# Performance work log

Measured on AMD Instinct MI355X. Metric: run time of the kernel, lower is better.

The kernel has to match this reference:

```python
import jax, jax.numpy as jnp
import numpy as np

N = 100000   # nodes
E = 1600000  # edges
IN = 512     # in_channels
H = 256      # hidden_channels
C = 40       # out_channels
BITS = 8     # INT8 fake quantization


def fake_quant(x, bits=BITS):
    """Symmetric per-tensor quantize-dequantize with straight-through estimator."""
    qmax = float(2 ** (bits - 1) - 1)
    scale = jnp.max(jnp.abs(x)) / qmax + 1e-12
    q = jnp.clip(jnp.round(x / scale), -qmax - 1.0, qmax) * scale
    # STE: forward = q, backward = identity
    return x + jax.lax.stop_gradient(q - x)


def quant_linear(x, w, b):
    # LinearQuantized: fake-quant inputs and weights, fp accumulate
    return fake_quant(x) @ fake_quant(w).T + b


def gcn_propagate(x, edge_index):
    """Symmetric-normalized sparse propagation: out = D^-1/2 A D^-1/2 x."""
    src, dst = edge_index[0], edge_index[1]
    deg = jax.ops.segment_sum(jnp.ones((E,), x.dtype), dst, num_segments=N)
    dinv = jnp.where(deg > 0, jax.lax.rsqrt(jnp.maximum(deg, 1.0)), 0.0)
    coef = dinv[src] * dinv[dst]                     # [E]
    msgs = x[src] * coef[:, None]                    # [E, C]
    return jax.ops.segment_sum(msgs, dst, num_segments=N)  # [N, C]


def setup_inputs() -> dict:
    key = jax.random.key(0)
    ks = jax.random.split(key, 6)
    x = jax.random.normal(ks[0], (N, IN), jnp.float32)
    edge_index = jax.random.randint(ks[1], (2, E), 0, N, dtype=jnp.int32)
    w1 = jax.random.normal(ks[2], (H, IN), jnp.float32) * (1.0 / np.sqrt(IN))
    b1 = jnp.zeros((H,), jnp.float32)
    w2 = jax.random.normal(ks[3], (C, H), jnp.float32) * (1.0 / np.sqrt(H))
    b2 = jnp.zeros((C,), jnp.float32)
    return {"x": x, "edge_index": edge_index, "w1": w1, "b1": b1, "w2": w2, "b2": b2}


def reference(x, edge_index, w1, b1, w2, b2):
    # dropout: identity in eval mode
    h = jax.nn.relu(quant_linear(x, w1, b1))         # [N, H]
    z = quant_linear(h, w2, b2)                      # [N, C]
    z = gcn_propagate(z, edge_index)                 # [N, C]
    return jax.nn.log_softmax(z, axis=1)
```

## Files before the change

kernel.cpp:

```cpp
#include <hip/hip_runtime.h>
#include <hip/hip_bf16.h>
#include <stdint.h>
#include <stddef.h>

#define NN   100000
#define NE   1600000
#define INC  512
#define HID  256
#define OC   40
#define OCP  48

#define LDK  72
#define LDB2 264

#define NBKT ((NN + 255) / 256)

typedef __bf16 bf16_t;
typedef __bf16 bf16x8 __attribute__((ext_vector_type(8)));
typedef __bf16 bf16x4 __attribute__((ext_vector_type(4)));
typedef float  f32x4  __attribute__((ext_vector_type(4)));

__device__ unsigned g_amax_bits[4];
__device__ float    g_dinv[NN];
__device__ bf16_t   g_qw1[HID * INC];
__device__ bf16_t   g_qw2[OCP * HID];
__device__ float    g_h[(size_t)NN * HID];
__device__ float    g_z[(size_t)NN * OC];
__device__ unsigned g_chist[NBKT];
__device__ unsigned g_cstart[NBKT + 1];
__device__ unsigned g_ccur[NBKT];
__device__ uint2    g_bin[NE];
__device__ unsigned g_rowstart[NN + 1];
__device__ int      g_csr_src[NE];

__device__ __forceinline__ bf16_t quant1(float v, float rs) {
    return (bf16_t)fminf(fmaxf(rintf(v * rs), -128.0f), 127.0f);
}

__global__ void init_kernel() {
    int idx = blockIdx.x * blockDim.x + threadIdx.x;
    int stride = gridDim.x * blockDim.x;
    for (int i = idx; i < NBKT; i += stride) g_chist[i] = 0u;
    for (int i = idx; i < OCP * HID; i += stride) g_qw2[i] = (bf16_t)0.0f;
    if (idx < 4) g_amax_bits[idx] = 0u;
}

__global__ void chist_kernel(const int* __restrict__ ei) {
    const int* dst = ei + NE;
    __shared__ unsigned hist[NBKT];
    int t = threadIdx.x;
    for (int i = t; i < NBKT; i += 256) hist[i] = 0u;
    __syncthreads();
    int idx = blockIdx.x * 256 + t;
    int stride = gridDim.x * 256;
    for (int e = idx; e < NE; e += stride) atomicAdd(&hist[dst[e] >> 8], 1u);
    __syncthreads();
    for (int i = t; i < NBKT; i += 256) {
        unsigned c = hist[i];
        if (c) atomicAdd(&g_chist[i], c);
    }
}

__global__ void cscan_kernel() {
    int t = threadIdx.x;
    unsigned v = (t < NBKT) ? g_chist[t] : 0u;
    int lane = t & 63, wv = t >> 6;
    unsigned sc = v;
#pragma unroll
    for (int off = 1; off < 64; off <<= 1) {
        unsigned n = __shfl_up(sc, off, 64);
        if (lane >= off) sc += n;
    }
    __shared__ unsigned ws[8];
    if (lane == 63) ws[wv] = sc;
    __syncthreads();
    unsigned woff = 0;
    for (int w = 0; w < 8; w++) if (w < wv) woff += ws[w];
    unsigned excl = woff + sc - v;
    if (t < NBKT) { g_cstart[t] = excl; g_ccur[t] = excl; }
    if (t == 0) g_cstart[NBKT] = NE;
}

#define BIN_BLOCKS 200
#define BIN_EPB    (NE / BIN_BLOCKS)
__global__ void bin_kernel(const int* __restrict__ ei) {
    const int* srcp = ei;
    const int* dstp = ei + NE;
    __shared__ unsigned hist[NBKT];
    __shared__ unsigned base[NBKT];
    int t = threadIdx.x;
    int e0 = blockIdx.x * BIN_EPB, e1 = e0 + BIN_EPB;
    for (int i = t; i < NBKT; i += 256) hist[i] = 0u;
    __syncthreads();
    for (int e = e0 + t; e < e1; e += 256) atomicAdd(&hist[dstp[e] >> 8], 1u);
    __syncthreads();
    for (int i = t; i < NBKT; i += 256) {
        unsigned c = hist[i];
        base[i] = c ? atomicAdd(&g_ccur[i], c) : 0u;
        hist[i] = 0u;
    }
    __syncthreads();
    for (int e = e0 + t; e < e1; e += 256) {
        int d = dstp[e], s = srcp[e];
        int b = d >> 8;
        unsigned r = atomicAdd(&hist[b], 1u);
        g_bin[base[b] + r] = make_uint2((unsigned)s, (unsigned)d);
    }
}

__global__ void local_kernel() {
    int b = blockIdx.x, t = threadIdx.x;
    unsigned e0 = g_cstart[b], e1 = g_cstart[b + 1];
    __shared__ unsigned hist[256];
    __shared__ unsigned curs[256];
    __shared__ unsigned wsum[4];
    hist[t] = 0u;
    __syncthreads();
    for (unsigned e = e0 + t; e < e1; e += 256) atomicAdd(&hist[g_bin[e].y & 255], 1u);
    __syncthreads();
    unsigned v = hist[t];
    int lane = t & 63, wv = t >> 6;
    unsigned sc = v;
#pragma unroll
    for (int off = 1; off < 64; off <<= 1) {
        unsigned n = __shfl_up(sc, off, 64);
        if (lane >= off) sc += n;
    }
    if (lane == 63) wsum[wv] = sc;
    __syncthreads();
    unsigned woff = 0;
    for (int w = 0; w < 4; w++) if (w < wv) woff += wsum[w];
    unsigned excl = woff + sc - v;
    int node = b * 256 + t;
    if (node < NN) {
        g_rowstart[node] = e0 + excl;
        g_dinv[node] = v ? rsqrtf((float)v) : 0.0f;
    }
    if (b == 0 && t == 0) g_rowstart[NN] = NE;
    curs[t] = excl;
    __syncthreads();
    for (unsigned e = e0 + t; e < e1; e += 256) {
        uint2 ed = g_bin[e];
        unsigned r = atomicAdd(&curs[ed.y & 255], 1u);
        g_csr_src[e0 + r] = (int)ed.x;
    }
}

__global__ void absmax_kernel(const float* __restrict__ src, int n4, int slot) {
    int idx = blockIdx.x * blockDim.x + threadIdx.x;
    int stride = gridDim.x * blockDim.x;
    const f32x4* s4 = (const f32x4*)src;
    float m = 0.0f;
    for (int i = idx; i < n4; i += stride) {
        f32x4 v = s4[i];
        m = fmaxf(m, fmaxf(fmaxf(fabsf(v.x), fabsf(v.y)),
                           fmaxf(fabsf(v.z), fabsf(v.w))));
    }
#pragma unroll
    for (int off = 32; off > 0; off >>= 1) m = fmaxf(m, __shfl_xor(m, off, 64));
    __shared__ float sm[4];
    if ((threadIdx.x & 63) == 0) sm[threadIdx.x >> 6] = m;
    __syncthreads();
    if (threadIdx.x == 0) {
        float mm = fmaxf(fmaxf(sm[0], sm[1]), fmaxf(sm[2], sm[3]));
        atomicMax(&g_amax_bits[slot], __float_as_uint(mm));
    }
}

__global__ void quantw_kernel(const float* __restrict__ src, int n4, int slot, int which) {
    bf16_t* dst = which ? g_qw2 : g_qw1;
    float rs = 1.0f / (__uint_as_float(g_amax_bits[slot]) / 127.0f + 1e-12f);
    int idx = blockIdx.x * blockDim.x + threadIdx.x;
    int stride = gridDim.x * blockDim.x;
    const f32x4* s4 = (const f32x4*)src;
    bf16x4* d4 = (bf16x4*)dst;
    for (int i = idx; i < n4; i += stride) {
        f32x4 v = s4[i];
        bf16x4 o;
        o[0] = quant1(v.x, rs); o[1] = quant1(v.y, rs);
        o[2] = quant1(v.z, rs); o[3] = quant1(v.w, rs);
        d4[i] = o;
    }
}

__launch_bounds__(256)
__global__ void gemm1_kernel(const float* __restrict__ x, const float* __restrict__ b1) {
    __shared__ bf16_t lA[128 * LDK];
    __shared__ bf16_t lB[128 * LDK];
    int t = threadIdx.x;
    int mtile = blockIdx.x >> 1, ntile = blockIdx.x & 1;
    int lane = t & 63, wv = t >> 6;
    int quad = lane >> 4, l16 = lane & 15;
    int mq = wv >> 1, nq = wv & 1;

    float scale_x = __uint_as_float(g_amax_bits[0]) / 127.0f + 1e-12f;
    float rs = 1.0f / scale_x;

    int srow = t >> 3;
    int sch  = t & 7;

    const float*  xbase[4];
    const bf16_t* wbase[4];
#pragma unroll
    for (int p = 0; p < 4; p++) {
        int gr = mtile * 128 + p * 32 + srow; if (gr >= NN) gr = NN - 1;
        xbase[p] = x + (size_t)gr * INC + sch * 8;
        wbase[p] = g_qw1 + (size_t)(ntile * 128 + p * 32 + srow) * INC + sch * 8;
    }

    f32x4 acc[4][4] = {};
#pragma unroll 1
    for (int kit = 0; kit < 8; kit++) {
        __syncthreads();
#pragma unroll
        for (int p = 0; p < 4; p++) {
            int row = p * 32 + srow;
            f32x4 v0 = *(const f32x4*)(xbase[p] + kit * 64);
            f32x4 v1 = *(const f32x4*)(xbase[p] + kit * 64 + 4);
            bf16x8 bb = *(const bf16x8*)(wbase[p] + kit * 64);
            bf16x8 o;
            o[0] = quant1(v0.x, rs); o[1] = quant1(v0.y, rs);
            o[2] = quant1(v0.z, rs); o[3] = quant1(v0.w, rs);
            o[4] = quant1(v1.x, rs); o[5] = quant1(v1.y, rs);
            o[6] = quant1(v1.z, rs); o[7] = quant1(v1.w, rs);
            *(bf16x8*)(lA + row * LDK + sch * 8) = o;
            *(bf16x8*)(lB + row * LDK + sch * 8) = bb;
        }
        __syncthreads();
#pragma unroll
        for (int k32 = 0; k32 < 2; k32++) {
            int cs = (k32 * 4 + quad) * 8;
            bf16x8 a[4], b[4];
#pragma unroll
            for (int i = 0; i < 4; i++)
                a[i] = *(const bf16x8*)(lA + (mq * 64 + i * 16 + l16) * LDK + cs);
#pragma unroll
            for (int j = 0; j < 4; j++)
                b[j] = *(const bf16x8*)(lB + (nq * 64 + j * 16 + l16) * LDK + cs);
#pragma unroll
            for (int i = 0; i < 4; i++)
#pragma unroll
                for (int j = 0; j < 4; j++)
                    acc[i][j] = __builtin_amdgcn_mfma_f32_16x16x32_bf16(a[i], b[j], acc[i][j], 0, 0, 0);
        }
    }
    float s = scale_x * (__uint_as_float(g_amax_bits[1]) / 127.0f + 1e-12f);
    float lmax = 0.0f;
#pragma unroll
    for (int j = 0; j < 4; j++) {
        int col = ntile * 128 + nq * 64 + j * 16 + l16;
        float bias = b1[col];
#pragma unroll
        for (int i = 0; i < 4; i++) {
#pragma unroll
            for (int r = 0; r < 4; r++) {
                int grow = mtile * 128 + mq * 64 + i * 16 + quad * 4 + r;
                float v = fmaxf(s * acc[i][j][r] + bias, 0.0f);
                lmax = fmaxf(lmax, v);
                if (grow < NN) g_h[(size_t)grow * HID + col] = v;
            }
        }
    }
#pragma unroll
    for (int off = 32; off > 0; off >>= 1) lmax = fmaxf(lmax, __shfl_xor(lmax, off, 64));
    if (lane == 0) atomicMax(&g_amax_bits[3], __float_as_uint(lmax));
}

__launch_bounds__(256)
__global__ void gemm2_kernel(const float* __restrict__ b2) {
    __shared__ bf16_t lB2[OCP * LDB2];
    __shared__ bf16_t lA2[128 * LDK];
    int t = threadIdx.x;
    int mtile = blockIdx.x;
    int lane = t & 63, wv = t >> 6;
    int quad = lane >> 4, l16 = lane & 15;

#pragma unroll
    for (int p = 0; p < 6; p++) {
        int ci = p * 256 + t;
        int row = ci >> 5, ch = ci & 31;
        *(bf16x8*)(lB2 + row * LDB2 + ch * 8) =
            *(const bf16x8*)(g_qw2 + row * 256 + ch * 8);
    }

    float scale_h = __uint_as_float(g_amax_bits[3]) / 127.0f + 1e-12f;
    float rs = 1.0f / scale_h;
    int srow = t >> 3, sch = t & 7;
    const float* hbase[4];
#pragma unroll
    for (int p = 0; p < 4; p++) {
        int gr = mtile * 128 + p * 32 + srow; if (gr >= NN) gr = NN - 1;
        hbase[p] = g_h + (size_t)gr * HID + sch * 8;
    }

    f32x4 acc[2][3] = {};
#pragma unroll 1
    for (int kit = 0; kit < 4; kit++) {
        if (kit) __syncthreads();
#pragma unroll
        for (int p = 0; p < 4; p++) {
            int row = p * 32 + srow;
            f32x4 v0 = *(const f32x4*)(hbase[p] + kit * 64);
            f32x4 v1 = *(const f32x4*)(hbase[p] + kit * 64 + 4);
            bf16x8 o;
            o[0] = quant1(v0.x, rs); o[1] = quant1(v0.y, rs);
            o[2] = quant1(v0.z, rs); o[3] = quant1(v0.w, rs);
            o[4] = quant1(v1.x, rs); o[5] = quant1(v1.y, rs);
            o[6] = quant1(v1.z, rs); o[7] = quant1(v1.w, rs);
            *(bf16x8*)(lA2 + row * LDK + sch * 8) = o;
        }
        __syncthreads();
#pragma unroll
        for (int k32 = 0; k32 < 2; k32++) {
            int csA = (k32 * 4 + quad) * 8;
            int chB = (kit * 8 + k32 * 4 + quad) * 8;
            bf16x8 a[2], b[3];
#pragma unroll
            for (int i = 0; i < 2; i++)
                a[i] = *(const bf16x8*)(lA2 + (wv * 32 + i * 16 + l16) * LDK + csA);
#pragma unroll
            for (int j = 0; j < 3; j++)
                b[j] = *(const bf16x8*)(lB2 + (j * 16 + l16) * LDB2 + chB);
#pragma unroll
            for (int i = 0; i < 2; i++)
#pragma unroll
                for (int j = 0; j < 3; j++)
                    acc[i][j] = __builtin_amdgcn_mfma_f32_16x16x32_bf16(a[i], b[j], acc[i][j], 0, 0, 0);
        }
    }
    float s = scale_h * (__uint_as_float(g_amax_bits[2]) / 127.0f + 1e-12f);
#pragma unroll
    for (int j = 0; j < 3; j++) {
        int col = j * 16 + l16;
        float bias = (col < OC) ? b2[col] : 0.0f;
#pragma unroll
        for (int i = 0; i < 2; i++) {
#pragma unroll
            for (int r = 0; r < 4; r++) {
                int grow = mtile * 128 + wv * 32 + i * 16 + quad * 4 + r;
                if (col < OC && grow < NN)
                    g_z[(size_t)grow * OC + col] = s * acc[i][j][r] + bias;
            }
        }
    }
}

__launch_bounds__(256)
__global__ void gather_kernel(float* __restrict__ out) {
    int node = (blockIdx.x * 256 + threadIdx.x) >> 6;
    int lane = threadIdx.x & 63;
    if (node >= NN) return;
    unsigned e0 = g_rowstart[node], e1 = g_rowstart[node + 1];
    float dinvd = g_dinv[node];
    float acc = 0.0f;
    unsigned e = e0;
    for (; e + 2 <= e1; e += 2) {
        int s0 = g_csr_src[e], s1 = g_csr_src[e + 1];
        float c0 = g_dinv[s0] * dinvd;
        float c1 = g_dinv[s1] * dinvd;
        float z0 = (lane < OC) ? g_z[(size_t)s0 * OC + lane] : 0.0f;
        float z1 = (lane < OC) ? g_z[(size_t)s1 * OC + lane] : 0.0f;
        acc += z0 * c0 + z1 * c1;
    }
    if (e < e1) {
        int s0 = g_csr_src[e];
        float c0 = g_dinv[s0] * dinvd;
        float z0 = (lane < OC) ? g_z[(size_t)s0 * OC + lane] : 0.0f;
        acc += z0 * c0;
    }
    float m = (lane < OC) ? acc : -1e30f;
#pragma unroll
    for (int off = 32; off > 0; off >>= 1) m = fmaxf(m, __shfl_xor(m, off, 64));
    float ex = (lane < OC) ? __expf(acc - m) : 0.0f;
    float ssum = ex;
#pragma unroll
    for (int off = 32; off > 0; off >>= 1) ssum += __shfl_xor(ssum, off, 64);
    float lg = __logf(ssum);
    if (lane < OC) out[(size_t)node * OC + lane] = acc - m - lg;
}

extern "C" void kernel_launch(void* const* d_in, const int* in_sizes, int n_in,
                              void* d_out, int out_size, void* d_ws, size_t ws_size,
                              hipStream_t stream) {
    const float* x  = (const float*)d_in[0];
    const int*   ei = (const int*)d_in[1];
    const float* w1 = (const float*)d_in[2];
    const float* b1 = (const float*)d_in[3];
    const float* w2 = (const float*)d_in[4];
    const float* b2 = (const float*)d_in[5];
    float* out = (float*)d_out;
    (void)d_ws; (void)ws_size; (void)in_sizes; (void)n_in; (void)out_size;

    init_kernel<<<1024, 256, 0, stream>>>();
    chist_kernel<<<128, 256, 0, stream>>>(ei);
    cscan_kernel<<<1, 512, 0, stream>>>();
    bin_kernel<<<BIN_BLOCKS, 256, 0, stream>>>(ei);
    local_kernel<<<NBKT, 256, 0, stream>>>();
    absmax_kernel<<<2048, 256, 0, stream>>>(x,  (NN * INC) / 4, 0);
    absmax_kernel<<<128, 256, 0, stream>>>(w1, (HID * INC) / 4, 1);
    absmax_kernel<<<10, 256, 0, stream>>>(w2,  (OC * HID) / 4, 2);
    quantw_kernel<<<128, 256, 0, stream>>>(w1, (HID * INC) / 4, 1, 0);
    quantw_kernel<<<10, 256, 0, stream>>>(w2,  (OC * HID) / 4, 2, 1);
    gemm1_kernel<<<((NN + 127) / 128) * 2, 256, 0, stream>>>(x, b1);
    gemm2_kernel<<<(NN + 127) / 128, 256, 0, stream>>>(b2);
    gather_kernel<<<(NN + 3) / 4, 256, 0, stream>>>(out);
}
```

Baseline: 642.5 us.

## Double-buffer LDS tiles and prefetch next K-slice in gemm1

Splits the gemm1 shared-memory A and B tiles into two buffers and loads the next K iteration's x and weight data into registers while the current tile is consumed by MFMA. This removes one barrier per iteration and is meant to hide global-load latency behind compute. In exchange it doubles the LDS footprint (about 72KB per block), which may reduce occupancy, and it raises register pressure from the prefetch registers.

Measured after the change: 634.8 us. Within noise of the previous version (-1.2%).

```diff
diff --git a/kernel.cpp b/kernel.cpp
--- a/kernel.cpp
+++ b/kernel.cpp
@@ -185,8 +185,8 @@
 
 __launch_bounds__(256)
 __global__ void gemm1_kernel(const float* __restrict__ x, const float* __restrict__ b1) {
-    __shared__ bf16_t lA[128 * LDK];
-    __shared__ bf16_t lB[128 * LDK];
+    __shared__ bf16_t lA[2][128 * LDK];
+    __shared__ bf16_t lB[2][128 * LDK];
     int t = threadIdx.x;
     int mtile = blockIdx.x >> 1, ntile = blockIdx.x & 1;
     int lane = t & 63, wv = t >> 6;
@@ -208,23 +208,36 @@
         wbase[p] = g_qw1 + (size_t)(ntile * 128 + p * 32 + srow) * INC + sch * 8;
     }
 
+    f32x4 av[4][2]; bf16x8 bv[4];
+#pragma unroll
+    for (int p = 0; p < 4; p++) {
+        av[p][0] = *(const f32x4*)(xbase[p]);
+        av[p][1] = *(const f32x4*)(xbase[p] + 4);
+        bv[p]    = *(const bf16x8*)(wbase[p]);
+    }
+
     f32x4 acc[4][4] = {};
 #pragma unroll 1
     for (int kit = 0; kit < 8; kit++) {
-        __syncthreads();
+        int bs = kit & 1;
 #pragma unroll
         for (int p = 0; p < 4; p++) {
             int row = p * 32 + srow;
-            f32x4 v0 = *(const f32x4*)(xbase[p] + kit * 64);
-            f32x4 v1 = *(const f32x4*)(xbase[p] + kit * 64 + 4);
-            bf16x8 bb = *(const bf16x8*)(wbase[p] + kit * 64);
             bf16x8 o;
-            o[0] = quant1(v0.x, rs); o[1] = quant1(v0.y, rs);
-            o[2] = quant1(v0.z, rs); o[3] = quant1(v0.w, rs);
-            o[4] = quant1(v1.x, rs); o[5] = quant1(v1.y, rs);
-            o[6] = quant1(v1.z, rs); o[7] = quant1(v1.w, rs);
-            *(bf16x8*)(lA + row * LDK + sch * 8) = o;
-            *(bf16x8*)(lB + row * LDK + sch * 8) = bb;
+            o[0] = quant1(av[p][0].x, rs); o[1] = quant1(av[p][0].y, rs);
+            o[2] = quant1(av[p][0].z, rs); o[3] = quant1(av[p][0].w, rs);
+            o[4] = quant1(av[p][1].x, rs); o[5] = quant1(av[p][1].y, rs);
+            o[6] = quant1(av[p][1].z, rs); o[7] = quant1(av[p][1].w, rs);
+            *(bf16x8*)(lA[bs] + row * LDK + sch * 8) = o;
+            *(bf16x8*)(lB[bs] + row * LDK + sch * 8) = bv[p];
+        }
+        if (kit + 1 < 8) {
+#pragma unroll
+            for (int p = 0; p < 4; p++) {
+                av[p][0] = *(const f32x4*)(xbase[p] + (kit + 1) * 64);
+                av[p][1] = *(const f32x4*)(xbase[p] + (kit + 1) * 64 + 4);
+                bv[p]    = *(const bf16x8*)(wbase[p] + (kit + 1) * 64);
+            }
         }
         __syncthreads();
 #pragma unroll
@@ -233,10 +246,10 @@
             bf16x8 a[4], b[4];
 #pragma unroll
             for (int i = 0; i < 4; i++)
-                a[i] = *(const bf16x8*)(lA + (mq * 64 + i * 16 + l16) * LDK + cs);
+                a[i] = *(const bf16x8*)(lA[bs] + (mq * 64 + i * 16 + l16) * LDK + cs);
 #pragma unroll
             for (int j = 0; j < 4; j++)
-                b[j] = *(const bf16x8*)(lB + (nq * 64 + j * 16 + l16) * LDK + cs);
+                b[j] = *(const bf16x8*)(lB[bs] + (nq * 64 + j * 16 + l16) * LDK + cs);
 #pragma unroll
             for (int i = 0; i < 4; i++)
 #pragma unroll
```
